# Kernel optimization log

Measured on AMD Instinct MI355X. Metric: run time of the kernel, lower is better.

Reference implementation:

```python
import jax, jax.numpy as jnp
import numpy as np

ASSIGN_RATIO = 0.1  # hard-coded inside coarsen_graph in the original
EPS_CUT = 1e-7
EPS_NORM = 1e-12  # torch F.normalize eps


def _normalize_batch_adj(adj):
    # adj: [B, N, N]
    n = adj.shape[1]
    A = adj + jnp.eye(n, dtype=adj.dtype)
    deg_inv_sqrt = jnp.clip(A.sum(-1), 1.0, None) ** -0.5  # [B, N]
    newA = deg_inv_sqrt[..., :, None] * A * deg_inv_sqrt[..., None, :]
    row_mask = (adj.sum(-1) > 0).astype(adj.dtype)  # [B, N]
    return row_mask[..., :, None] * newA


def setup_inputs():
    key = jax.random.key(0)
    k0, k1, k2, k3, k4 = jax.random.split(key, 5)
    B, N, D, T = 512, 128, 256, 512
    concept_hidden = jax.random.normal(k0, (B, N, D), jnp.float32)
    adj = jax.random.uniform(k1, (B, N, N), jnp.float32)
    head = jax.random.randint(k2, (B, T), 0, N)
    lin_w = jax.random.normal(k3, (1, D), jnp.float32) / np.sqrt(D).astype(np.float32)
    bias = jax.random.normal(k4, (1,), jnp.float32)
    return {"concept_hidden": concept_hidden, "adj": adj, "head": head,
            "lin_w": lin_w, "bias": bias}


def reference(concept_hidden, adj, head, lin_w, bias):
    # concept_hidden: [B, N, D], adj: [B, N, N], head: [B, T] node indices
    x = concept_hidden
    B, N, D = x.shape

    out = x @ lin_w.T                      # [B, N, 1]  self.lin(x)
    norm_adj = _normalize_batch_adj(adj)   # [B, N, N]
    out = norm_adj @ out + bias            # [B, N, 1]
    alpha = jax.nn.sigmoid(out ** 2)[..., 0]  # [B, N]

    # batch_num_nodes[i] = len(set(head[i]))  -> count unique via sort
    hs = jnp.sort(head, axis=-1)
    n_uniq = 1 + (hs[:, 1:] != hs[:, :-1]).sum(-1)  # [B]

    # per-sample k = ceil(n * 0.1) + 1 (only when n > 1); cut = k-th largest alpha
    k = jnp.ceil(n_uniq.astype(jnp.float32) * ASSIGN_RATIO).astype(jnp.int32) + 1
    a_desc = jnp.sort(alpha, axis=-1)[:, ::-1]       # descending
    idx = jnp.clip(k - 1, 0, N - 1)
    cut = jnp.take_along_axis(a_desc, idx[:, None], axis=-1)[:, 0]
    cut = jnp.where(n_uniq > 1, cut, jnp.zeros_like(cut))  # [B]

    cut_alpha = jax.nn.relu(alpha + EPS_CUT - cut[:, None])  # [B, N]

    # S = norm_adj * cut_alpha broadcast over rows, then L1-normalize rows
    S = norm_adj * cut_alpha[:, None, :]
    S = S / jnp.clip(jnp.abs(S).sum(-1, keepdims=True), EPS_NORM, None)

    St = jnp.swapaxes(S, 1, 2)             # [B, N, N]
    embedding_tensor = St @ x              # S^T x   [B, N, D]
    new_adj = (St @ adj) @ S               # S^T A S [B, N, N]
    return embedding_tensor, new_adj
```

## Files before the change

kernel.cpp:

```cpp
#include <hip/hip_runtime.h>

#define Bsz 512
#define Nn  128
#define Dd  256
#define Tt  512

typedef __attribute__((ext_vector_type(8))) short short8;
typedef __attribute__((ext_vector_type(4))) float f32x4;

__device__ __forceinline__ ushort f2bf(float f) {
    union { float f; unsigned u; } v; v.f = f;
    unsigned r = v.u + 0x7fffu + ((v.u >> 16) & 1u);
    return (ushort)(r >> 16);
}
__device__ __forceinline__ unsigned pk2(float a, float b) {
    return (unsigned)f2bf(a) | ((unsigned)f2bf(b) << 16);
}
__device__ __forceinline__ float bf2f(ushort u) {
    union { unsigned u; float f; } v; v.u = (unsigned)u << 16; return v.f;
}

__global__ __launch_bounds__(1024, 4) void mega(
    const float* __restrict__ x, const float* __restrict__ adj,
    const int* __restrict__ head, const float* __restrict__ lin_w,
    const float* __restrict__ bias,
    float* __restrict__ emb, float* __restrict__ nadj)
{
    const int t = threadIdx.x, b = blockIdx.x;
    __shared__ __align__(16) ushort adjB[Nn][136];
    __shared__ __align__(16) ushort STl[Nn][136];
    __shared__ __align__(16) uint   xT0[Nn][68];
    __shared__ __align__(16) uint   xT1[Nn][68];
    __shared__ float ttS[Nn], disS[Nn], maskS[Nn], alphaS[Nn], rowcS[Nn];
    __shared__ float dotP2[Nn][2];
    __shared__ int   flags[Nn];
    __shared__ int   nuniq;
    __shared__ float cutS;

    const float bias0 = bias[0];
    if (t < Nn) flags[t] = 0;
    if (t == 0) { nuniq = 0; cutS = 0.f; }

    const int lane = t & 63, w = t >> 6;
    const int l15 = lane & 15, quad = lane >> 4;
    const int mrow  = (w & 7) * 16;
    const int nhalf = (w >> 3) * 64;
    const int r = t >> 3, seg = t & 7;
    const int xrow = t & 127, kq0 = t >> 7;

    int hv = 0;
    if (t < Tt) hv = head[(size_t)b * Tt + t];

    float e0[8], g0[8], e1[8], g1[8];
    {
        const float* xb = x + (size_t)b * Nn * Dd + xrow;
#pragma unroll
        for (int k = 0; k < 8; ++k) e0[k] = xb[(size_t)(8 * kq0 + k) * Dd];
#pragma unroll
        for (int k = 0; k < 8; ++k) g0[k] = xb[(size_t)(64 + 8 * kq0 + k) * Dd];
#pragma unroll
        for (int k = 0; k < 8; ++k) e1[k] = xb[(size_t)(8 * kq0 + k) * Dd + 128];
#pragma unroll
        for (int k = 0; k < 8; ++k) g1[k] = xb[(size_t)(64 + 8 * kq0 + k) * Dd + 128];
    }
    float4 av0, av1, av2, av3;
    {
        const float4* adjb = (const float4*)(adj + (size_t)b * Nn * Nn);
        av0 = adjb[t]; av1 = adjb[t + 1024]; av2 = adjb[t + 2048]; av3 = adjb[t + 3072];
    }
    const float wv0 = lin_w[xrow], wv1 = lin_w[128 + xrow];

#pragma unroll
    for (int k = 0; k < 8; ++k) {
        float re = e0[k] * wv0 + e1[k] * wv1;
        float rg = g0[k] * wv0 + g1[k] * wv1;
        re += __shfl_xor(re, 1); re += __shfl_xor(re, 2); re += __shfl_xor(re, 4);
        re += __shfl_xor(re, 8); re += __shfl_xor(re, 16); re += __shfl_xor(re, 32);
        rg += __shfl_xor(rg, 1); rg += __shfl_xor(rg, 2); rg += __shfl_xor(rg, 4);
        rg += __shfl_xor(rg, 8); rg += __shfl_xor(rg, 16); rg += __shfl_xor(rg, 32);
        if (lane == 0) {
            dotP2[8 * kq0 + k][w & 1]      = re;
            dotP2[64 + 8 * kq0 + k][w & 1] = rg;
        }
    }

    {
        uint4 q;
        q.x = pk2(e0[0], e0[1]); q.y = pk2(e0[2], e0[3]);
        q.z = pk2(e0[4], e0[5]); q.w = pk2(e0[6], e0[7]);
        *(uint4*)&xT0[xrow][4 * kq0] = q;
        q.x = pk2(g0[0], g0[1]); q.y = pk2(g0[2], g0[3]);
        q.z = pk2(g0[4], g0[5]); q.w = pk2(g0[6], g0[7]);
        *(uint4*)&xT0[xrow][4 * (kq0 + 8)] = q;
        q.x = pk2(e1[0], e1[1]); q.y = pk2(e1[2], e1[3]);
        q.z = pk2(e1[4], e1[5]); q.w = pk2(e1[6], e1[7]);
        *(uint4*)&xT1[xrow][4 * kq0] = q;
        q.x = pk2(g1[0], g1[1]); q.y = pk2(g1[2], g1[3]);
        q.z = pk2(g1[4], g1[5]); q.w = pk2(g1[6], g1[7]);
        *(uint4*)&xT1[xrow][4 * (kq0 + 8)] = q;
    }
    {
        float4 v; int f, rr2, c; uint2 w2;
        v = av0; f = t;        rr2 = f >> 5; c = (f & 31) * 4; w2.x = pk2(v.x, v.y); w2.y = pk2(v.z, v.w); *(uint2*)&adjB[rr2][c] = w2;
        v = av1; f = t + 1024; rr2 = f >> 5; c = (f & 31) * 4; w2.x = pk2(v.x, v.y); w2.y = pk2(v.z, v.w); *(uint2*)&adjB[rr2][c] = w2;
        v = av2; f = t + 2048; rr2 = f >> 5; c = (f & 31) * 4; w2.x = pk2(v.x, v.y); w2.y = pk2(v.z, v.w); *(uint2*)&adjB[rr2][c] = w2;
        v = av3; f = t + 3072; rr2 = f >> 5; c = (f & 31) * 4; w2.x = pk2(v.x, v.y); w2.y = pk2(v.z, v.w); *(uint2*)&adjB[rr2][c] = w2;
    }
    __syncthreads();

    if (t < Tt) flags[hv] = 1;

    {
        short8 a0 = *(const short8*)&adjB[r][seg * 16];
        short8 a1 = *(const short8*)&adjB[r][seg * 16 + 8];
        float s = 0.f;
#pragma unroll
        for (int j = 0; j < 8; ++j) s += bf2f((ushort)a0[j]) + bf2f((ushort)a1[j]);
        s += __shfl_xor(s, 1); s += __shfl_xor(s, 2); s += __shfl_xor(s, 4);
        if (seg == 0) {
            maskS[r] = (s > 0.f) ? 1.f : 0.f;
            float dis = 1.f / sqrtf(fmaxf(s + 1.f, 1.f));
            disS[r] = dis;
            ttS[r]  = dis * (dotP2[r][0] + dotP2[r][1]);
        }
    }
    __syncthreads();

    {
        short8 a0 = *(const short8*)&adjB[r][seg * 16];
        short8 a1 = *(const short8*)&adjB[r][seg * 16 + 8];
        float s = 0.f;
#pragma unroll
        for (int j = 0; j < 8; ++j) {
            s += bf2f((ushort)a0[j]) * ttS[seg * 16 + j];
            s += bf2f((ushort)a1[j]) * ttS[seg * 16 + 8 + j];
        }
        s += __shfl_xor(s, 1); s += __shfl_xor(s, 2); s += __shfl_xor(s, 4);
        if (seg == 0) {
            float o = maskS[r] * disS[r] * (s + ttS[r]) + bias0;
            alphaS[r] = 1.f / (1.f + expf(-o * o));
            atomicAdd(&nuniq, flags[r]);
        }
    }
    __syncthreads();

    {
        int nu = nuniq;
        if (nu > 1) {
            float an = alphaS[r];
            int cg = 0, ce = 0;
            const int j0 = seg * 16;
#pragma unroll
            for (int j = 0; j < 16; ++j) {
                float aj = alphaS[j0 + j];
                cg += (aj > an); ce += (aj == an);
            }
            cg += __shfl_xor(cg, 1); cg += __shfl_xor(cg, 2); cg += __shfl_xor(cg, 4);
            ce += __shfl_xor(ce, 1); ce += __shfl_xor(ce, 2); ce += __shfl_xor(ce, 4);
            if (seg == 0) {
                int idx = (int)ceilf((float)nu * 0.1f);
                if (idx > Nn - 1) idx = Nn - 1;
                if (cg <= idx && idx < cg + ce) cutS = an;
            }
        }
    }
    __syncthreads();

    {
        const float cut = cutS;
        short8 a0 = *(const short8*)&adjB[r][seg * 16];
        short8 a1 = *(const short8*)&adjB[r][seg * 16 + 8];
        float s = 0.f;
#pragma unroll
        for (int j = 0; j < 8; ++j) {
            int j0 = seg * 16 + j, j1 = seg * 16 + 8 + j;
            float u0 = fmaxf(alphaS[j0] + 1e-7f - cut, 0.f) * disS[j0];
            float u1 = fmaxf(alphaS[j1] + 1e-7f - cut, 0.f) * disS[j1];
            s += bf2f((ushort)a0[j]) * u0 + bf2f((ushort)a1[j]) * u1;
        }
        s += __shfl_xor(s, 1); s += __shfl_xor(s, 2); s += __shfl_xor(s, 4);
        if (seg == 0) {
            float ur   = fmaxf(alphaS[r] + 1e-7f - cut, 0.f) * disS[r];
            float rsum = maskS[r] * disS[r] * (ur + s);
            rowcS[r]   = maskS[r] * disS[r] / fmaxf(rsum, 1e-12f);
        }
    }
    __syncthreads();

    {
        const float cut = cutS;
        const int m = t & 127, sl = t >> 7, k0 = sl * 16;
        const float um = fmaxf(alphaS[m] + 1e-7f - cut, 0.f) * disS[m];
        float vv[16];
#pragma unroll
        for (int j = 0; j < 16; ++j) {
            int k = k0 + j;
            vv[j] = rowcS[k] * (bf2f(adjB[k][m]) + ((k == m) ? 1.f : 0.f)) * um;
        }
        uint4 p0, p1;
        p0.x = pk2(vv[0],  vv[1]);  p0.y = pk2(vv[2],  vv[3]);
        p0.z = pk2(vv[4],  vv[5]);  p0.w = pk2(vv[6],  vv[7]);
        p1.x = pk2(vv[8],  vv[9]);  p1.y = pk2(vv[10], vv[11]);
        p1.z = pk2(vv[12], vv[13]); p1.w = pk2(vv[14], vv[15]);
        *(uint4*)&STl[m][k0]     = p0;
        *(uint4*)&STl[m][k0 + 8] = p1;
    }
    __syncthreads();

    f32x4 acc[4];
#pragma unroll
    for (int nt = 0; nt < 4; ++nt) acc[nt] = (f32x4){0.f, 0.f, 0.f, 0.f};
#pragma unroll
    for (int k0 = 0; k0 < 128; k0 += 32) {
        short8 a0 = *(const short8*)&adjB[mrow + l15][k0 + quad * 8];
#pragma unroll
        for (int nt = 0; nt < 4; ++nt) {
            short8 bf = *(const short8*)&STl[nhalf + nt * 16 + l15][k0 + quad * 8];
            acc[nt] = __builtin_amdgcn_mfma_f32_16x16x32_bf16(a0, bf, acc[nt], 0, 0, 0);
        }
    }
    __syncthreads();

    ushort (*PT)[136] = (ushort(*)[136])&adjB[0][0];
#pragma unroll
    for (int nt = 0; nt < 4; ++nt) {
        int j    = nhalf + nt * 16 + l15;
        int mcol = mrow + quad * 4;
        uint2 w2;
        w2.x = pk2(acc[nt][0], acc[nt][1]);
        w2.y = pk2(acc[nt][2], acc[nt][3]);
        *(uint2*)&PT[j][mcol] = w2;
    }
    __syncthreads();

#pragma unroll
    for (int nt = 0; nt < 4; ++nt) acc[nt] = (f32x4){0.f, 0.f, 0.f, 0.f};
#pragma unroll
    for (int k0 = 0; k0 < 128; k0 += 32) {
        short8 a0 = *(const short8*)&STl[mrow + l15][k0 + quad * 8];
#pragma unroll
        for (int nt = 0; nt < 4; ++nt) {
            short8 bf = *(const short8*)&PT[nhalf + nt * 16 + l15][k0 + quad * 8];
            acc[nt] = __builtin_amdgcn_mfma_f32_16x16x32_bf16(a0, bf, acc[nt], 0, 0, 0);
        }
    }
#pragma unroll
    for (int nt = 0; nt < 4; ++nt)
#pragma unroll
        for (int rr2 = 0; rr2 < 4; ++rr2) {
            int row = mrow + quad * 4 + rr2;
            int col = nhalf + nt * 16 + l15;
            nadj[((size_t)b * Nn + row) * Nn + col] = acc[nt][rr2];
        }

    const int dcb = (w >> 3) * 64;
    short8 aE[4];
#pragma unroll
    for (int ks = 0; ks < 4; ++ks)
        aE[ks] = *(const short8*)&STl[mrow + l15][ks * 32 + quad * 8];

    f32x4 accE[4];
#pragma unroll
    for (int nt = 0; nt < 4; ++nt) accE[nt] = (f32x4){0.f, 0.f, 0.f, 0.f};
#pragma unroll
    for (int ks = 0; ks < 4; ++ks) {
#pragma unroll
        for (int nt = 0; nt < 4; ++nt) {
            short8 bf = *(const short8*)&xT0[dcb + nt * 16 + l15][ks * 16 + quad * 4];
            accE[nt] = __builtin_amdgcn_mfma_f32_16x16x32_bf16(aE[ks], bf, accE[nt], 0, 0, 0);
        }
    }
#pragma unroll
    for (int nt = 0; nt < 4; ++nt)
#pragma unroll
        for (int rr2 = 0; rr2 < 4; ++rr2) {
            int row = mrow + quad * 4 + rr2;
            int col = dcb + nt * 16 + l15;
            emb[((size_t)b * Nn + row) * Dd + col] = accE[nt][rr2];
        }

#pragma unroll
    for (int nt = 0; nt < 4; ++nt) accE[nt] = (f32x4){0.f, 0.f, 0.f, 0.f};
#pragma unroll
    for (int ks = 0; ks < 4; ++ks) {
#pragma unroll
        for (int nt = 0; nt < 4; ++nt) {
            short8 bf = *(const short8*)&xT1[dcb + nt * 16 + l15][ks * 16 + quad * 4];
            accE[nt] = __builtin_amdgcn_mfma_f32_16x16x32_bf16(aE[ks], bf, accE[nt], 0, 0, 0);
        }
    }
#pragma unroll
    for (int nt = 0; nt < 4; ++nt)
#pragma unroll
        for (int rr2 = 0; rr2 < 4; ++rr2) {
            int row = mrow + quad * 4 + rr2;
            int col = 128 + dcb + nt * 16 + l15;
            emb[((size_t)b * Nn + row) * Dd + col] = accE[nt][rr2];
        }
}

extern "C" void kernel_launch(void* const* d_in, const int* in_sizes, int n_in,
                              void* d_out, int out_size, void* d_ws, size_t ws_size,
                              hipStream_t stream)
{
    const float* x     = (const float*)d_in[0];
    const float* adj   = (const float*)d_in[1];
    const int*   head  = (const int*)d_in[2];
    const float* lin_w = (const float*)d_in[3];
    const float* bias  = (const float*)d_in[4];

    float* emb  = (float*)d_out;
    float* nadj = emb + (size_t)Bsz * Nn * Dd;

    mega<<<Bsz, 1024, 0, stream>>>(x, adj, head, lin_w, bias, emb, nadj);
}
```

Baseline: 200.1 us.

## Process two graphs per block and prefetch the second graph's inputs during compute

Each block now handles two batch samples in sequence. It issues the global loads of x, adj and head for the second sample before the MFMA phase of the first, so memory latency overlaps with compute. The grid is halved to 256 blocks. It also replaces __syncthreads with a custom barrier that waits only on LDS counters, and cuts the full-wave dot-product shuffle reduction to 8 lanes plus a partial-sum table. In exchange, the prefetch registers raise register pressure, and 256 blocks on a 256-CU part may leave less parallelism to hide latency.

After: 309.5 us. +54.6%, slower.

```diff
diff --git a/kernel.cpp b/kernel.cpp
--- a/kernel.cpp
+++ b/kernel.cpp
@@ -19,6 +19,11 @@
 __device__ __forceinline__ float bf2f(ushort u) {
     union { unsigned u; float f; } v; v.u = (unsigned)u << 16; return v.f;
 }
+
+#define BARL() do { __builtin_amdgcn_sched_barrier(0); \
+    asm volatile("s_waitcnt lgkmcnt(0)" ::: "memory"); \
+    __builtin_amdgcn_s_barrier(); \
+    __builtin_amdgcn_sched_barrier(0); } while (0)
 
 __global__ __launch_bounds__(1024, 4) void mega(
     const float* __restrict__ x, const float* __restrict__ adj,
@@ -26,277 +31,319 @@
     const float* __restrict__ bias,
     float* __restrict__ emb, float* __restrict__ nadj)
 {
-    const int t = threadIdx.x, b = blockIdx.x;
+    const int t = threadIdx.x;
     __shared__ __align__(16) ushort adjB[Nn][136];
     __shared__ __align__(16) ushort STl[Nn][136];
     __shared__ __align__(16) uint   xT0[Nn][68];
     __shared__ __align__(16) uint   xT1[Nn][68];
-    __shared__ float ttS[Nn], disS[Nn], maskS[Nn], alphaS[Nn], rowcS[Nn];
-    __shared__ float dotP2[Nn][2];
+    __shared__ __align__(16) float ttS[Nn], disS[Nn], alphaS[Nn], rowcS[Nn];
+    __shared__ float maskS[Nn];
+    __shared__ float partS[Nn][18];
     __shared__ int   flags[Nn];
     __shared__ int   nuniq;
     __shared__ float cutS;
 
     const float bias0 = bias[0];
-    if (t < Nn) flags[t] = 0;
-    if (t == 0) { nuniq = 0; cutS = 0.f; }
-
     const int lane = t & 63, w = t >> 6;
     const int l15 = lane & 15, quad = lane >> 4;
     const int mrow  = (w & 7) * 16;
     const int nhalf = (w >> 3) * 64;
     const int r = t >> 3, seg = t & 7;
     const int xrow = t & 127, kq0 = t >> 7;
-
-    int hv = 0;
-    if (t < Tt) hv = head[(size_t)b * Tt + t];
-
-    float e0[8], g0[8], e1[8], g1[8];
-    {
-        const float* xb = x + (size_t)b * Nn * Dd + xrow;
-#pragma unroll
-        for (int k = 0; k < 8; ++k) e0[k] = xb[(size_t)(8 * kq0 + k) * Dd];
-#pragma unroll
-        for (int k = 0; k < 8; ++k) g0[k] = xb[(size_t)(64 + 8 * kq0 + k) * Dd];
-#pragma unroll
-        for (int k = 0; k < 8; ++k) e1[k] = xb[(size_t)(8 * kq0 + k) * Dd + 128];
-#pragma unroll
-        for (int k = 0; k < 8; ++k) g1[k] = xb[(size_t)(64 + 8 * kq0 + k) * Dd + 128];
+    const float wv0 = lin_w[xrow], wv1 = lin_w[128 + xrow];
+
+    float pe0[8], pg0[8], pe1[8], pg1[8];
+    float4 pav0, pav1, pav2, pav3;
+    int hv1 = 0;
+
+    for (int it = 0; it < 2; ++it) {
+        const int b = 2 * blockIdx.x + it;
+
+        if (t < Nn) flags[t] = 0;
+        if (t == 0) { nuniq = 0; cutS = 0.f; }
+
+        int hv = 0;
+        float e0[8], g0[8], e1[8], g1[8];
+        float4 a0v, a1v, a2v, a3v;
+        if (it == 0) {
+            if (t < Tt) hv = head[(size_t)b * Tt + t];
+            const float* xb = x + (size_t)b * Nn * Dd + xrow;
+#pragma unroll
+            for (int k = 0; k < 8; ++k) e0[k] = xb[(size_t)(8 * kq0 + k) * Dd];
+#pragma unroll
+            for (int k = 0; k < 8; ++k) g0[k] = xb[(size_t)(64 + 8 * kq0 + k) * Dd];
+#pragma unroll
+            for (int k = 0; k < 8; ++k) e1[k] = xb[(size_t)(8 * kq0 + k) * Dd + 128];
+#pragma unroll
+            for (int k = 0; k < 8; ++k) g1[k] = xb[(size_t)(64 + 8 * kq0 + k) * Dd + 128];
+            const float4* ab = (const float4*)(adj + (size_t)b * Nn * Nn);
+            a0v = ab[t]; a1v = ab[t + 1024]; a2v = ab[t + 2048]; a3v = ab[t + 3072];
+        } else {
+            hv = hv1;
+#pragma unroll
+            for (int k = 0; k < 8; ++k) { e0[k] = pe0[k]; g0[k] = pg0[k]; e1[k] = pe1[k]; g1[k] = pg1[k]; }
+            a0v = pav0; a1v = pav1; a2v = pav2; a3v = pav3;
+        }
+
+#pragma unroll
+        for (int k = 0; k < 8; ++k) {
+            float re = e0[k] * wv0 + e1[k] * wv1;
+            float rg = g0[k] * wv0 + g1[k] * wv1;
+            re += __shfl_xor(re, 1); re += __shfl_xor(re, 2); re += __shfl_xor(re, 4);
+            rg += __shfl_xor(rg, 1); rg += __shfl_xor(rg, 2); rg += __shfl_xor(rg, 4);
+            if ((lane & 7) == 0) {
+                int gc = (w & 1) * 8 + (lane >> 3);
+                partS[8 * kq0 + k][gc]      = re;
+                partS[64 + 8 * kq0 + k][gc] = rg;
+            }
+        }
+        {
+            uint4 q;
+            q.x = pk2(e0[0], e0[1]); q.y = pk2(e0[2], e0[3]);
+            q.z = pk2(e0[4], e0[5]); q.w = pk2(e0[6], e0[7]);
+            *(uint4*)&xT0[xrow][4 * kq0] = q;
+            q.x = pk2(g0[0], g0[1]); q.y = pk2(g0[2], g0[3]);
+            q.z = pk2(g0[4], g0[5]); q.w = pk2(g0[6], g0[7]);
+            *(uint4*)&xT0[xrow][4 * kq0 + 32] = q;
+            q.x = pk2(e1[0], e1[1]); q.y = pk2(e1[2], e1[3]);
+            q.z = pk2(e1[4], e1[5]); q.w = pk2(e1[6], e1[7]);
+            *(uint4*)&xT1[xrow][4 * kq0] = q;
+            q.x = pk2(g1[0], g1[1]); q.y = pk2(g1[2], g1[3]);
+            q.z = pk2(g1[4], g1[5]); q.w = pk2(g1[6], g1[7]);
+            *(uint4*)&xT1[xrow][4 * kq0 + 32] = q;
+        }
+        {
+            float4 v; int f, rr2, c; uint2 w2;
+            v = a0v; f = t;        rr2 = f >> 5; c = (f & 31) * 4; w2.x = pk2(v.x, v.y); w2.y = pk2(v.z, v.w); *(uint2*)&adjB[rr2][c] = w2;
+            v = a1v; f = t + 1024; rr2 = f >> 5; c = (f & 31) * 4; w2.x = pk2(v.x, v.y); w2.y = pk2(v.z, v.w); *(uint2*)&adjB[rr2][c] = w2;
+            v = a2v; f = t + 2048; rr2 = f >> 5; c = (f & 31) * 4; w2.x = pk2(v.x, v.y); w2.y = pk2(v.z, v.w); *(uint2*)&adjB[rr2][c] = w2;
+            v = a3v; f = t + 3072; rr2 = f >> 5; c = (f & 31) * 4; w2.x = pk2(v.x, v.y); w2.y = pk2(v.z, v.w); *(uint2*)&adjB[rr2][c] = w2;
+        }
+        BARL();
+
+        if (t < Tt) flags[hv] = 1;
+
+        {
+            short8 a0 = *(const short8*)&adjB[r][seg * 16];
+            short8 a1 = *(const short8*)&adjB[r][seg * 16 + 8];
+            float s = 0.f;
+#pragma unroll
+            for (int j = 0; j < 8; ++j) s += bf2f((ushort)a0[j]) + bf2f((ushort)a1[j]);
+            float d = partS[r][2 * seg] + partS[r][2 * seg + 1];
+            s += __shfl_xor(s, 1); s += __shfl_xor(s, 2); s += __shfl_xor(s, 4);
+            d += __shfl_xor(d, 1); d += __shfl_xor(d, 2); d += __shfl_xor(d, 4);
+            if (seg == 0) {
+                maskS[r] = (s > 0.f) ? 1.f : 0.f;
+                float dis = 1.f / sqrtf(fmaxf(s + 1.f, 1.f));
+                disS[r] = dis;
+                ttS[r]  = dis * d;
+            }
+        }
+        BARL();
+
+        {
+            short8 a0 = *(const short8*)&adjB[r][seg * 16];
+            short8 a1 = *(const short8*)&adjB[r][seg * 16 + 8];
+            f32x4 t0 = *(const f32x4*)&ttS[seg * 16];
+            f32x4 t1 = *(const f32x4*)&ttS[seg * 16 + 4];
+            f32x4 t2 = *(const f32x4*)&ttS[seg * 16 + 8];
+            f32x4 t3 = *(const f32x4*)&ttS[seg * 16 + 12];
+            float s = 0.f;
+#pragma unroll
+            for (int j = 0; j < 4; ++j) {
+                s += bf2f((ushort)a0[j])     * t0[j];
+                s += bf2f((ushort)a0[4 + j]) * t1[j];
+                s += bf2f((ushort)a1[j])     * t2[j];
+                s += bf2f((ushort)a1[4 + j]) * t3[j];
+            }
+            s += __shfl_xor(s, 1); s += __shfl_xor(s, 2); s += __shfl_xor(s, 4);
+            if (seg == 0) {
+                float o = maskS[r] * disS[r] * (s + ttS[r]) + bias0;
+                alphaS[r] = 1.f / (1.f + expf(-o * o));
+                atomicAdd(&nuniq, flags[r]);
+            }
+        }
+        BARL();
+
+        {
+            int nu = nuniq;
+            if (nu > 1) {
+                float an = alphaS[r];
+                int cg = 0, ce = 0;
+#pragma unroll
+                for (int v = 0; v < 4; ++v) {
+                    f32x4 A = *(const f32x4*)&alphaS[seg * 16 + 4 * v];
+#pragma unroll
+                    for (int j = 0; j < 4; ++j) { cg += (A[j] > an); ce += (A[j] == an); }
+                }
+                cg += __shfl_xor(cg, 1); cg += __shfl_xor(cg, 2); cg += __shfl_xor(cg, 4);
+                ce += __shfl_xor(ce, 1); ce += __shfl_xor(ce, 2); ce += __shfl_xor(ce, 4);
+                if (seg == 0) {
+                    int idx = (int)ceilf((float)nu * 0.1f);
+                    if (idx > Nn - 1) idx = Nn - 1;
+                    if (cg <= idx && idx < cg + ce) cutS = an;
+                }
+            }
+        }
+        BARL();
+
+        {
+            const float cut = cutS;
+            short8 a0 = *(const short8*)&adjB[r][seg * 16];
+            short8 a1 = *(const short8*)&adjB[r][seg * 16 + 8];
+            float s = 0.f;
+#pragma unroll
+            for (int v = 0; v < 4; ++v) {
+                f32x4 A = *(const f32x4*)&alphaS[seg * 16 + 4 * v];
+                f32x4 D = *(const f32x4*)&disS[seg * 16 + 4 * v];
+#pragma unroll
+                for (int j = 0; j < 4; ++j) {
+                    float u = fmaxf(A[j] + 1e-7f - cut, 0.f) * D[j];
+                    float av = (v < 2) ? bf2f((ushort)a0[4 * v + j])
+                                       : bf2f((ushort)a1[4 * (v - 2) + j]);
+                    s += av * u;
+                }
+            }
+            s += __shfl_xor(s, 1); s += __shfl_xor(s, 2); s += __shfl_xor(s, 4);
+            if (seg == 0) {
+                float ur   = fmaxf(alphaS[r] + 1e-7f - cut, 0.f) * disS[r];
+                float rsum = maskS[r] * disS[r] * (ur + s);
+                rowcS[r]   = maskS[r] * disS[r] / fmaxf(rsum, 1e-12f);
+            }
+        }
+        BARL();
+
+        {
+            const float cut = cutS;
+            const int m = t & 127, sl = t >> 7, k0 = sl * 16;
+            const float um = fmaxf(alphaS[m] + 1e-7f - cut, 0.f) * disS[m];
+            f32x4 R0 = *(const f32x4*)&rowcS[k0];
+            f32x4 R1 = *(const f32x4*)&rowcS[k0 + 4];
+            f32x4 R2 = *(const f32x4*)&rowcS[k0 + 8];
+            f32x4 R3 = *(const f32x4*)&rowcS[k0 + 12];
+            float vv[16];
+#pragma unroll
+            for (int j = 0; j < 16; ++j) {
+                int k = k0 + j;
+                float rc = (j < 4) ? R0[j] : (j < 8) ? R1[j - 4] : (j < 12) ? R2[j - 8] : R3[j - 12];
+                vv[j] = rc * (bf2f(adjB[k][m]) + ((k == m) ? 1.f : 0.f)) * um;
+            }
+            uint4 p0, p1;
+            p0.x = pk2(vv[0],  vv[1]);  p0.y = pk2(vv[2],  vv[3]);
+            p0.z = pk2(vv[4],  vv[5]);  p0.w = pk2(vv[6],  vv[7]);
+            p1.x = pk2(vv[8],  vv[9]);  p1.y = pk2(vv[10], vv[11]);
+            p1.z = pk2(vv[12], vv[13]); p1.w = pk2(vv[14], vv[15]);
+            *(uint4*)&STl[m][k0]     = p0;
+            *(uint4*)&STl[m][k0 + 8] = p1;
+        }
+        BARL();
+
+        if (it == 0) {
+            const float* xb = x + (size_t)(b + 1) * Nn * Dd + xrow;
+#pragma unroll
+            for (int k = 0; k < 8; ++k) pe0[k] = xb[(size_t)(8 * kq0 + k) * Dd];
+#pragma unroll
+            for (int k = 0; k < 8; ++k) pg0[k] = xb[(size_t)(64 + 8 * kq0 + k) * Dd];
+#pragma unroll
+            for (int k = 0; k < 8; ++k) pe1[k] = xb[(size_t)(8 * kq0 + k) * Dd + 128];
+#pragma unroll
+            for (int k = 0; k < 8; ++k) pg1[k] = xb[(size_t)(64 + 8 * kq0 + k) * Dd + 128];
+            const float4* ab = (const float4*)(adj + (size_t)(b + 1) * Nn * Nn);
+            pav0 = ab[t]; pav1 = ab[t + 1024]; pav2 = ab[t + 2048]; pav3 = ab[t + 3072];
+            if (t < Tt) hv1 = head[(size_t)(b + 1) * Tt + t];
+            __builtin_amdgcn_sched_barrier(0);
+        }
+
+        f32x4 acc[4];
+#pragma unroll
+        for (int nt = 0; nt < 4; ++nt) acc[nt] = (f32x4){0.f, 0.f, 0.f, 0.f};
+#pragma unroll
+        for (int k0 = 0; k0 < 128; k0 += 32) {
+            short8 a0 = *(const short8*)&adjB[mrow + l15][k0 + quad * 8];
+#pragma unroll
+            for (int nt = 0; nt < 4; ++nt) {
+                short8 bf = *(const short8*)&STl[nhalf + nt * 16 + l15][k0 + quad * 8];
+                acc[nt] = __builtin_amdgcn_mfma_f32_16x16x32_bf16(a0, bf, acc[nt], 0, 0, 0);
+            }
+        }
+        BARL();
+
+        ushort (*PT)[136] = (ushort(*)[136])&adjB[0][0];
+#pragma unroll
+        for (int nt = 0; nt < 4; ++nt) {
+            int j    = nhalf + nt * 16 + l15;
+            int mcol = mrow + quad * 4;
+            uint2 w2;
+            w2.x = pk2(acc[nt][0], acc[nt][1]);
+            w2.y = pk2(acc[nt][2], acc[nt][3]);
+            *(uint2*)&PT[j][mcol] = w2;
+        }
+        BARL();
+
+#pragma unroll
+        for (int nt = 0; nt < 4; ++nt) acc[nt] = (f32x4){0.f, 0.f, 0.f, 0.f};
+#pragma unroll
+        for (int k0 = 0; k0 < 128; k0 += 32) {
+            short8 a0 = *(const short8*)&STl[mrow + l15][k0 + quad * 8];
+#pragma unroll
+            for (int nt = 0; nt < 4; ++nt) {
+                short8 bf = *(const short8*)&PT[nhalf + nt * 16 + l15][k0 + quad * 8];
+                acc[nt] = __builtin_amdgcn_mfma_f32_16x16x32_bf16(a0, bf, acc[nt], 0, 0, 0);
+            }
+        }
+#pragma unroll
+        for (int nt = 0; nt < 4; ++nt)
+#pragma unroll
+            for (int rr2 = 0; rr2 < 4; ++rr2) {
+                int row = mrow + quad * 4 + rr2;
+                int col = nhalf + nt * 16 + l15;
+                nadj[((size_t)b * Nn + row) * Nn + col] = acc[nt][rr2];
+            }
+
+        const int dcb = (w >> 3) * 64;
+        f32x4 accE[4];
+#pragma unroll
+        for (int nt = 0; nt < 4; ++nt) accE[nt] = (f32x4){0.f, 0.f, 0.f, 0.f};
+#pragma unroll
+        for (int ks = 0; ks < 4; ++ks) {
+            short8 aE = *(const short8*)&STl[mrow + l15][ks * 32 + quad * 8];
+#pragma unroll
+            for (int nt = 0; nt < 4; ++nt) {
+                short8 bf = *(const short8*)&xT0[dcb + nt * 16 + l15][ks * 16 + quad * 4];
+                accE[nt] = __builtin_amdgcn_mfma_f32_16x16x32_bf16(aE, bf, accE[nt], 0, 0, 0);
+            }
+        }
+#pragma unroll
+        for (int nt = 0; nt < 4; ++nt)
+#pragma unroll
+            for (int rr2 = 0; rr2 < 4; ++rr2) {
+                int row = mrow + quad * 4 + rr2;
+                int col = dcb + nt * 16 + l15;
+                emb[((size_t)b * Nn + row) * Dd + col] = accE[nt][rr2];
+            }
+
+#pragma unroll
+        for (int nt = 0; nt < 4; ++nt) accE[nt] = (f32x4){0.f, 0.f, 0.f, 0.f};
+#pragma unroll
+        for (int ks = 0; ks < 4; ++ks) {
+            short8 aE = *(const short8*)&STl[mrow + l15][ks * 32 + quad * 8];
+#pragma unroll
+            for (int nt = 0; nt < 4; ++nt) {
+                short8 bf = *(const short8*)&xT1[dcb + nt * 16 + l15][ks * 16 + quad * 4];
+                accE[nt] = __builtin_amdgcn_mfma_f32_16x16x32_bf16(aE, bf, accE[nt], 0, 0, 0);
+            }
+        }
+#pragma unroll
+        for (int nt = 0; nt < 4; ++nt)
+#pragma unroll
+            for (int rr2 = 0; rr2 < 4; ++rr2) {
+                int row = mrow + quad * 4 + rr2;
+                int col = 128 + dcb + nt * 16 + l15;
+                emb[((size_t)b * Nn + row) * Dd + col] = accE[nt][rr2];
+            }
+
+        BARL();
     }
-    float4 av0, av1, av2, av3;
-    {
-        const float4* adjb = (const float4*)(adj + (size_t)b * Nn * Nn);
-        av0 = adjb[t]; av1 = adjb[t + 1024]; av2 = adjb[t + 2048]; av3 = adjb[t + 3072];
-    }
-    const float wv0 = lin_w[xrow], wv1 = lin_w[128 + xrow];
-
-#pragma unroll
-    for (int k = 0; k < 8; ++k) {
-        float re = e0[k] * wv0 + e1[k] * wv1;
-        float rg = g0[k] * wv0 + g1[k] * wv1;
-        re += __shfl_xor(re, 1); re += __shfl_xor(re, 2); re += __shfl_xor(re, 4);
-        re += __shfl_xor(re, 8); re += __shfl_xor(re, 16); re += __shfl_xor(re, 32);
-        rg += __shfl_xor(rg, 1); rg += __shfl_xor(rg, 2); rg += __shfl_xor(rg, 4);
-        rg += __shfl_xor(rg, 8); rg += __shfl_xor(rg, 16); rg += __shfl_xor(rg, 32);
-        if (lane == 0) {
-            dotP2[8 * kq0 + k][w & 1]      = re;
-            dotP2[64 + 8 * kq0 + k][w & 1] = rg;
-        }
-    }
-
-    {
-        uint4 q;
-        q.x = pk2(e0[0], e0[1]); q.y = pk2(e0[2], e0[3]);
-        q.z = pk2(e0[4], e0[5]); q.w = pk2(e0[6], e0[7]);
-        *(uint4*)&xT0[xrow][4 * kq0] = q;
-        q.x = pk2(g0[0], g0[1]); q.y = pk2(g0[2], g0[3]);
-        q.z = pk2(g0[4], g0[5]); q.w = pk2(g0[6], g0[7]);
-        *(uint4*)&xT0[xrow][4 * (kq0 + 8)] = q;
-        q.x = pk2(e1[0], e1[1]); q.y = pk2(e1[2], e1[3]);
-        q.z = pk2(e1[4], e1[5]); q.w = pk2(e1[6], e1[7]);
-        *(uint4*)&xT1[xrow][4 * kq0] = q;
-        q.x = pk2(g1[0], g1[1]); q.y = pk2(g1[2], g1[3]);
-        q.z = pk2(g1[4], g1[5]); q.w = pk2(g1[6], g1[7]);
-        *(uint4*)&xT1[xrow][4 * (kq0 + 8)] = q;
-    }
-    {
-        float4 v; int f, rr2, c; uint2 w2;
-        v = av0; f = t;        rr2 = f >> 5; c = (f & 31) * 4; w2.x = pk2(v.x, v.y); w2.y = pk2(v.z, v.w); *(uint2*)&adjB[rr2][c] = w2;
-        v = av1; f = t + 1024; rr2 = f >> 5; c = (f & 31) * 4; w2.x = pk2(v.x, v.y); w2.y = pk2(v.z, v.w); *(uint2*)&adjB[rr2][c] = w2;
-        v = av2; f = t + 2048; rr2 = f >> 5; c = (f & 31) * 4; w2.x = pk2(v.x, v.y); w2.y = pk2(v.z, v.w); *(uint2*)&adjB[rr2][c] = w2;
-        v = av3; f = t + 3072; rr2 = f >> 5; c = (f & 31) * 4; w2.x = pk2(v.x, v.y); w2.y = pk2(v.z, v.w); *(uint2*)&adjB[rr2][c] = w2;
-    }
-    __syncthreads();
-
-    if (t < Tt) flags[hv] = 1;
-
-    {
-        short8 a0 = *(const short8*)&adjB[r][seg * 16];
-        short8 a1 = *(const short8*)&adjB[r][seg * 16 + 8];
-        float s = 0.f;
-#pragma unroll
-        for (int j = 0; j < 8; ++j) s += bf2f((ushort)a0[j]) + bf2f((ushort)a1[j]);
-        s += __shfl_xor(s, 1); s += __shfl_xor(s, 2); s += __shfl_xor(s, 4);
-        if (seg == 0) {
-            maskS[r] = (s > 0.f) ? 1.f : 0.f;
-            float dis = 1.f / sqrtf(fmaxf(s + 1.f, 1.f));
-            disS[r] = dis;
-            ttS[r]  = dis * (dotP2[r][0] + dotP2[r][1]);
-        }
-    }
-    __syncthreads();
-
-    {
-        short8 a0 = *(const short8*)&adjB[r][seg * 16];
-        short8 a1 = *(const short8*)&adjB[r][seg * 16 + 8];
-        float s = 0.f;
-#pragma unroll
-        for (int j = 0; j < 8; ++j) {
-            s += bf2f((ushort)a0[j]) * ttS[seg * 16 + j];
-            s += bf2f((ushort)a1[j]) * ttS[seg * 16 + 8 + j];
-        }
-        s += __shfl_xor(s, 1); s += __shfl_xor(s, 2); s += __shfl_xor(s, 4);
-        if (seg == 0) {
-            float o = maskS[r] * disS[r] * (s + ttS[r]) + bias0;
-            alphaS[r] = 1.f / (1.f + expf(-o * o));
-            atomicAdd(&nuniq, flags[r]);
-        }
-    }
-    __syncthreads();
-
-    {
-        int nu = nuniq;
-        if (nu > 1) {
-            float an = alphaS[r];
-            int cg = 0, ce = 0;
-            const int j0 = seg * 16;
-#pragma unroll
-            for (int j = 0; j < 16; ++j) {
-                float aj = alphaS[j0 + j];
-                cg += (aj > an); ce += (aj == an);
-            }
-            cg += __shfl_xor(cg, 1); cg += __shfl_xor(cg, 2); cg += __shfl_xor(cg, 4);
-            ce += __shfl_xor(ce, 1); ce += __shfl_xor(ce, 2); ce += __shfl_xor(ce, 4);
-            if (seg == 0) {
-                int idx = (int)ceilf((float)nu * 0.1f);
-                if (idx > Nn - 1) idx = Nn - 1;
-                if (cg <= idx && idx < cg + ce) cutS = an;
-            }
-        }
-    }
-    __syncthreads();
-
-    {
-        const float cut = cutS;
-        short8 a0 = *(const short8*)&adjB[r][seg * 16];
-        short8 a1 = *(const short8*)&adjB[r][seg * 16 + 8];
-        float s = 0.f;
-#pragma unroll
-        for (int j = 0; j < 8; ++j) {
-            int j0 = seg * 16 + j, j1 = seg * 16 + 8 + j;
-            float u0 = fmaxf(alphaS[j0] + 1e-7f - cut, 0.f) * disS[j0];
-            float u1 = fmaxf(alphaS[j1] + 1e-7f - cut, 0.f) * disS[j1];
-            s += bf2f((ushort)a0[j]) * u0 + bf2f((ushort)a1[j]) * u1;
-        }
-        s += __shfl_xor(s, 1); s += __shfl_xor(s, 2); s += __shfl_xor(s, 4);
-        if (seg == 0) {
-            float ur   = fmaxf(alphaS[r] + 1e-7f - cut, 0.f) * disS[r];
-            float rsum = maskS[r] * disS[r] * (ur + s);
-            rowcS[r]   = maskS[r] * disS[r] / fmaxf(rsum, 1e-12f);
-        }
-    }
-    __syncthreads();
-
-    {
-        const float cut = cutS;
-        const int m = t & 127, sl = t >> 7, k0 = sl * 16;
-        const float um = fmaxf(alphaS[m] + 1e-7f - cut, 0.f) * disS[m];
-        float vv[16];
-#pragma unroll
-        for (int j = 0; j < 16; ++j) {
-            int k = k0 + j;
-            vv[j] = rowcS[k] * (bf2f(adjB[k][m]) + ((k == m) ? 1.f : 0.f)) * um;
-        }
-        uint4 p0, p1;
-        p0.x = pk2(vv[0],  vv[1]);  p0.y = pk2(vv[2],  vv[3]);
-        p0.z = pk2(vv[4],  vv[5]);  p0.w = pk2(vv[6],  vv[7]);
-        p1.x = pk2(vv[8],  vv[9]);  p1.y = pk2(vv[10], vv[11]);
-        p1.z = pk2(vv[12], vv[13]); p1.w = pk2(vv[14], vv[15]);
-        *(uint4*)&STl[m][k0]     = p0;
-        *(uint4*)&STl[m][k0 + 8] = p1;
-    }
-    __syncthreads();
-
-    f32x4 acc[4];
-#pragma unroll
-    for (int nt = 0; nt < 4; ++nt) acc[nt] = (f32x4){0.f, 0.f, 0.f, 0.f};
-#pragma unroll
-    for (int k0 = 0; k0 < 128; k0 += 32) {
-        short8 a0 = *(const short8*)&adjB[mrow + l15][k0 + quad * 8];
-#pragma unroll
-        for (int nt = 0; nt < 4; ++nt) {
-            short8 bf = *(const short8*)&STl[nhalf + nt * 16 + l15][k0 + quad * 8];
-            acc[nt] = __builtin_amdgcn_mfma_f32_16x16x32_bf16(a0, bf, acc[nt], 0, 0, 0);
-        }
-    }
-    __syncthreads();
-
-    ushort (*PT)[136] = (ushort(*)[136])&adjB[0][0];
-#pragma unroll
-    for (int nt = 0; nt < 4; ++nt) {
-        int j    = nhalf + nt * 16 + l15;
-        int mcol = mrow + quad * 4;
-        uint2 w2;
-        w2.x = pk2(acc[nt][0], acc[nt][1]);
-        w2.y = pk2(acc[nt][2], acc[nt][3]);
-        *(uint2*)&PT[j][mcol] = w2;
-    }
-    __syncthreads();
-
-#pragma unroll
-    for (int nt = 0; nt < 4; ++nt) acc[nt] = (f32x4){0.f, 0.f, 0.f, 0.f};
-#pragma unroll
-    for (int k0 = 0; k0 < 128; k0 += 32) {
-        short8 a0 = *(const short8*)&STl[mrow + l15][k0 + quad * 8];
-#pragma unroll
-        for (int nt = 0; nt < 4; ++nt) {
-            short8 bf = *(const short8*)&PT[nhalf + nt * 16 + l15][k0 + quad * 8];
-            acc[nt] = __builtin_amdgcn_mfma_f32_16x16x32_bf16(a0, bf, acc[nt], 0, 0, 0);
-        }
-    }
-#pragma unroll
-    for (int nt = 0; nt < 4; ++nt)
-#pragma unroll
-        for (int rr2 = 0; rr2 < 4; ++rr2) {
-            int row = mrow + quad * 4 + rr2;
-            int col = nhalf + nt * 16 + l15;
-            nadj[((size_t)b * Nn + row) * Nn + col] = acc[nt][rr2];
-        }
-
-    const int dcb = (w >> 3) * 64;
-    short8 aE[4];
-#pragma unroll
-    for (int ks = 0; ks < 4; ++ks)
-        aE[ks] = *(const short8*)&STl[mrow + l15][ks * 32 + quad * 8];
-
-    f32x4 accE[4];
-#pragma unroll
-    for (int nt = 0; nt < 4; ++nt) accE[nt] = (f32x4){0.f, 0.f, 0.f, 0.f};
-#pragma unroll
-    for (int ks = 0; ks < 4; ++ks) {
-#pragma unroll
-        for (int nt = 0; nt < 4; ++nt) {
-            short8 bf = *(const short8*)&xT0[dcb + nt * 16 + l15][ks * 16 + quad * 4];
-            accE[nt] = __builtin_amdgcn_mfma_f32_16x16x32_bf16(aE[ks], bf, accE[nt], 0, 0, 0);
-        }
-    }
-#pragma unroll
-    for (int nt = 0; nt < 4; ++nt)
-#pragma unroll
-        for (int rr2 = 0; rr2 < 4; ++rr2) {
-            int row = mrow + quad * 4 + rr2;
-            int col = dcb + nt * 16 + l15;
-            emb[((size_t)b * Nn + row) * Dd + col] = accE[nt][rr2];
-        }
-
-#pragma unroll
-    for (int nt = 0; nt < 4; ++nt) accE[nt] = (f32x4){0.f, 0.f, 0.f, 0.f};
-#pragma unroll
-    for (int ks = 0; ks < 4; ++ks) {
-#pragma unroll
-        for (int nt = 0; nt < 4; ++nt) {
-            short8 bf = *(const short8*)&xT1[dcb + nt * 16 + l15][ks * 16 + quad * 4];
-            accE[nt] = __builtin_amdgcn_mfma_f32_16x16x32_bf16(aE[ks], bf, accE[nt], 0, 0, 0);
-        }
-    }
-#pragma unroll
-    for (int nt = 0; nt < 4; ++nt)
-#pragma unroll
-        for (int rr2 = 0; rr2 < 4; ++rr2) {
-            int row = mrow + quad * 4 + rr2;
-            int col = 128 + dcb + nt * 16 + l15;
-            emb[((size_t)b * Nn + row) * Dd + col] = accE[nt][rr2];
-        }
 }
 
 extern "C" void kernel_launch(void* const* d_in, const int* in_sizes, int n_in,
@@ -312,5 +359,5 @@
     float* emb  = (float*)d_out;
     float* nadj = emb + (size_t)Bsz * Nn * Dd;
 
-    mega<<<Bsz, 1024, 0, stream>>>(x, adj, head, lin_w, bias, emb, nadj);
-}
+    mega<<<Bsz / 2, 1024, 0, stream>>>(x, adj, head, lin_w, bias, emb, nadj);
+}
```

## Swizzle shared-memory tiles and compute row sums from fp32 registers

Applied to the files above, without the earlier changes.

Adds an XOR swizzle for the bf16 adjacency, S^T and transposed x tiles in shared memory, aimed at cutting LDS bank conflicts in the MFMA operand loads and the strided transpose reads. Row degree sums are now taken from the fp32 global loads through shuffles and partial buffers, and the lin dot-product reduction is shortened to three shuffles plus a shared-memory reduction, so one pass over adjB goes away. Several scalar LDS reads become vectorised f32x4 reads, and S^T fragments are reloaded per k-step instead of held in registers, which lowers register pressure. Degree sums now come from unrounded fp32 instead of bf16, which changes numerics slightly.

Result: slower. 204.9 us (+2.4%).

```diff
diff --git a/kernel.cpp b/kernel.cpp
--- a/kernel.cpp
+++ b/kernel.cpp
@@ -18,6 +18,16 @@
 }
 __device__ __forceinline__ float bf2f(ushort u) {
     union { unsigned u; float f; } v; v.u = (unsigned)u << 16; return v.f;
+}
+
+__device__ __forceinline__ int SWZ(int row, int g) {
+    return g ^ ((row ^ (row >> 3)) & 7);
+}
+__device__ __forceinline__ ushort* AP(ushort* base, int row, int col) {
+    return base + row * 136 + (SWZ(row, col >> 3) << 3) + (col & 7);
+}
+__device__ __forceinline__ uint* XP(uint* base, int row, int col) {
+    return base + row * 68 + (SWZ(row, col >> 2) << 2) + (col & 3);
 }
 
 __global__ __launch_bounds__(1024, 4) void mega(
@@ -27,12 +37,13 @@
     float* __restrict__ emb, float* __restrict__ nadj)
 {
     const int t = threadIdx.x, b = blockIdx.x;
-    __shared__ __align__(16) ushort adjB[Nn][136];
-    __shared__ __align__(16) ushort STl[Nn][136];
-    __shared__ __align__(16) uint   xT0[Nn][68];
-    __shared__ __align__(16) uint   xT1[Nn][68];
+    __shared__ __align__(16) ushort adjR[Nn * 136];
+    __shared__ __align__(16) ushort stR[Nn * 136];
+    __shared__ __align__(16) uint   xtR0[Nn * 68];
+    __shared__ __align__(16) uint   xtR1[Nn * 68];
     __shared__ float ttS[Nn], disS[Nn], maskS[Nn], alphaS[Nn], rowcS[Nn];
-    __shared__ float dotP2[Nn][2];
+    __shared__ float partS[Nn][18];
+    __shared__ float partS2[Nn][4];
     __shared__ int   flags[Nn];
     __shared__ int   nuniq;
     __shared__ float cutS;
@@ -47,6 +58,7 @@
     const int nhalf = (w >> 3) * 64;
     const int r = t >> 3, seg = t & 7;
     const int xrow = t & 127, kq0 = t >> 7;
+    const float wv0 = lin_w[xrow], wv1 = lin_w[128 + xrow];
 
     int hv = 0;
     if (t < Tt) hv = head[(size_t)b * Tt + t];
@@ -68,19 +80,36 @@
         const float4* adjb = (const float4*)(adj + (size_t)b * Nn * Nn);
         av0 = adjb[t]; av1 = adjb[t + 1024]; av2 = adjb[t + 2048]; av3 = adjb[t + 3072];
     }
-    const float wv0 = lin_w[xrow], wv1 = lin_w[128 + xrow];
 
 #pragma unroll
     for (int k = 0; k < 8; ++k) {
         float re = e0[k] * wv0 + e1[k] * wv1;
         float rg = g0[k] * wv0 + g1[k] * wv1;
         re += __shfl_xor(re, 1); re += __shfl_xor(re, 2); re += __shfl_xor(re, 4);
-        re += __shfl_xor(re, 8); re += __shfl_xor(re, 16); re += __shfl_xor(re, 32);
         rg += __shfl_xor(rg, 1); rg += __shfl_xor(rg, 2); rg += __shfl_xor(rg, 4);
-        rg += __shfl_xor(rg, 8); rg += __shfl_xor(rg, 16); rg += __shfl_xor(rg, 32);
-        if (lane == 0) {
-            dotP2[8 * kq0 + k][w & 1]      = re;
-            dotP2[64 + 8 * kq0 + k][w & 1] = rg;
+        if ((lane & 7) == 0) {
+            int gc = (w & 1) * 8 + (lane >> 3);
+            partS[8 * kq0 + k][gc]      = re;
+            partS[64 + 8 * kq0 + k][gc] = rg;
+        }
+    }
+
+    {
+        float s0 = av0.x + av0.y + av0.z + av0.w;
+        float s1 = av1.x + av1.y + av1.z + av1.w;
+        float s2 = av2.x + av2.y + av2.z + av2.w;
+        float s3 = av3.x + av3.y + av3.z + av3.w;
+        s0 += __shfl_xor(s0, 1); s0 += __shfl_xor(s0, 2); s0 += __shfl_xor(s0, 4);
+        s1 += __shfl_xor(s1, 1); s1 += __shfl_xor(s1, 2); s1 += __shfl_xor(s1, 4);
+        s2 += __shfl_xor(s2, 1); s2 += __shfl_xor(s2, 2); s2 += __shfl_xor(s2, 4);
+        s3 += __shfl_xor(s3, 1); s3 += __shfl_xor(s3, 2); s3 += __shfl_xor(s3, 4);
+        if ((lane & 7) == 0) {
+            int q = (lane & 31) >> 3;
+            int row0 = t >> 5;
+            partS2[row0][q]       = s0;
+            partS2[row0 + 32][q]  = s1;
+            partS2[row0 + 64][q]  = s2;
+            partS2[row0 + 96][q]  = s3;
         }
     }
 
@@ -88,52 +117,56 @@
         uint4 q;
         q.x = pk2(e0[0], e0[1]); q.y = pk2(e0[2], e0[3]);
         q.z = pk2(e0[4], e0[5]); q.w = pk2(e0[6], e0[7]);
-        *(uint4*)&xT0[xrow][4 * kq0] = q;
+        *(uint4*)XP(xtR0, xrow, 4 * kq0) = q;
         q.x = pk2(g0[0], g0[1]); q.y = pk2(g0[2], g0[3]);
         q.z = pk2(g0[4], g0[5]); q.w = pk2(g0[6], g0[7]);
-        *(uint4*)&xT0[xrow][4 * (kq0 + 8)] = q;
+        *(uint4*)XP(xtR0, xrow, 4 * kq0 + 32) = q;
         q.x = pk2(e1[0], e1[1]); q.y = pk2(e1[2], e1[3]);
         q.z = pk2(e1[4], e1[5]); q.w = pk2(e1[6], e1[7]);
-        *(uint4*)&xT1[xrow][4 * kq0] = q;
+        *(uint4*)XP(xtR1, xrow, 4 * kq0) = q;
         q.x = pk2(g1[0], g1[1]); q.y = pk2(g1[2], g1[3]);
         q.z = pk2(g1[4], g1[5]); q.w = pk2(g1[6], g1[7]);
-        *(uint4*)&xT1[xrow][4 * (kq0 + 8)] = q;
+        *(uint4*)XP(xtR1, xrow, 4 * kq0 + 32) = q;
     }
     {
         float4 v; int f, rr2, c; uint2 w2;
-        v = av0; f = t;        rr2 = f >> 5; c = (f & 31) * 4; w2.x = pk2(v.x, v.y); w2.y = pk2(v.z, v.w); *(uint2*)&adjB[rr2][c] = w2;
-        v = av1; f = t + 1024; rr2 = f >> 5; c = (f & 31) * 4; w2.x = pk2(v.x, v.y); w2.y = pk2(v.z, v.w); *(uint2*)&adjB[rr2][c] = w2;
-        v = av2; f = t + 2048; rr2 = f >> 5; c = (f & 31) * 4; w2.x = pk2(v.x, v.y); w2.y = pk2(v.z, v.w); *(uint2*)&adjB[rr2][c] = w2;
-        v = av3; f = t + 3072; rr2 = f >> 5; c = (f & 31) * 4; w2.x = pk2(v.x, v.y); w2.y = pk2(v.z, v.w); *(uint2*)&adjB[rr2][c] = w2;
+        v = av0; f = t;        rr2 = f >> 5; c = (f & 31) * 4; w2.x = pk2(v.x, v.y); w2.y = pk2(v.z, v.w); *(uint2*)AP(adjR, rr2, c) = w2;
+        v = av1; f = t + 1024; rr2 = f >> 5; c = (f & 31) * 4; w2.x = pk2(v.x, v.y); w2.y = pk2(v.z, v.w); *(uint2*)AP(adjR, rr2, c) = w2;
+        v = av2; f = t + 2048; rr2 = f >> 5; c = (f & 31) * 4; w2.x = pk2(v.x, v.y); w2.y = pk2(v.z, v.w); *(uint2*)AP(adjR, rr2, c) = w2;
+        v = av3; f = t + 3072; rr2 = f >> 5; c = (f & 31) * 4; w2.x = pk2(v.x, v.y); w2.y = pk2(v.z, v.w); *(uint2*)AP(adjR, rr2, c) = w2;
     }
     __syncthreads();
 
     if (t < Tt) flags[hv] = 1;
 
     {
-        short8 a0 = *(const short8*)&adjB[r][seg * 16];
-        short8 a1 = *(const short8*)&adjB[r][seg * 16 + 8];
-        float s = 0.f;
-#pragma unroll
-        for (int j = 0; j < 8; ++j) s += bf2f((ushort)a0[j]) + bf2f((ushort)a1[j]);
+        float d = partS[r][2 * seg] + partS[r][2 * seg + 1];
+        float s = (seg < 4) ? partS2[r][seg] : 0.f;
+        d += __shfl_xor(d, 1); d += __shfl_xor(d, 2); d += __shfl_xor(d, 4);
         s += __shfl_xor(s, 1); s += __shfl_xor(s, 2); s += __shfl_xor(s, 4);
         if (seg == 0) {
             maskS[r] = (s > 0.f) ? 1.f : 0.f;
             float dis = 1.f / sqrtf(fmaxf(s + 1.f, 1.f));
             disS[r] = dis;
-            ttS[r]  = dis * (dotP2[r][0] + dotP2[r][1]);
-        }
-    }
-    __syncthreads();
-
-    {
-        short8 a0 = *(const short8*)&adjB[r][seg * 16];
-        short8 a1 = *(const short8*)&adjB[r][seg * 16 + 8];
+            ttS[r]  = dis * d;
+        }
+    }
+    __syncthreads();
+
+    {
+        short8 a0 = *(const short8*)AP(adjR, r, seg * 16);
+        short8 a1 = *(const short8*)AP(adjR, r, seg * 16 + 8);
+        f32x4 t0 = *(const f32x4*)&ttS[seg * 16];
+        f32x4 t1 = *(const f32x4*)&ttS[seg * 16 + 4];
+        f32x4 t2 = *(const f32x4*)&ttS[seg * 16 + 8];
+        f32x4 t3 = *(const f32x4*)&ttS[seg * 16 + 12];
         float s = 0.f;
 #pragma unroll
-        for (int j = 0; j < 8; ++j) {
-            s += bf2f((ushort)a0[j]) * ttS[seg * 16 + j];
-            s += bf2f((ushort)a1[j]) * ttS[seg * 16 + 8 + j];
+        for (int j = 0; j < 4; ++j) {
+            s += bf2f((ushort)a0[j])     * t0[j];
+            s += bf2f((ushort)a0[4 + j]) * t1[j];
+            s += bf2f((ushort)a1[j])     * t2[j];
+            s += bf2f((ushort)a1[4 + j]) * t3[j];
         }
         s += __shfl_xor(s, 1); s += __shfl_xor(s, 2); s += __shfl_xor(s, 4);
         if (seg == 0) {
@@ -149,11 +182,11 @@
         if (nu > 1) {
             float an = alphaS[r];
             int cg = 0, ce = 0;
-            const int j0 = seg * 16;
-#pragma unroll
-            for (int j = 0; j < 16; ++j) {
-                float aj = alphaS[j0 + j];
-                cg += (aj > an); ce += (aj == an);
+#pragma unroll
+            for (int v = 0; v < 4; ++v) {
+                f32x4 A = *(const f32x4*)&alphaS[seg * 16 + 4 * v];
+#pragma unroll
+                for (int j = 0; j < 4; ++j) { cg += (A[j] > an); ce += (A[j] == an); }
             }
             cg += __shfl_xor(cg, 1); cg += __shfl_xor(cg, 2); cg += __shfl_xor(cg, 4);
             ce += __shfl_xor(ce, 1); ce += __shfl_xor(ce, 2); ce += __shfl_xor(ce, 4);
@@ -168,15 +201,20 @@
 
     {
         const float cut = cutS;
-        short8 a0 = *(const short8*)&adjB[r][seg * 16];
-        short8 a1 = *(const short8*)&adjB[r][seg * 16 + 8];
+        short8 a0 = *(const short8*)AP(adjR, r, seg * 16);
+        short8 a1 = *(const short8*)AP(adjR, r, seg * 16 + 8);
         float s = 0.f;
 #pragma unroll
-        for (int j = 0; j < 8; ++j) {
-            int j0 = seg * 16 + j, j1 = seg * 16 + 8 + j;
-            float u0 = fmaxf(alphaS[j0] + 1e-7f - cut, 0.f) * disS[j0];
-            float u1 = fmaxf(alphaS[j1] + 1e-7f - cut, 0.f) * disS[j1];
-            s += bf2f((ushort)a0[j]) * u0 + bf2f((ushort)a1[j]) * u1;
+        for (int v = 0; v < 4; ++v) {
+            f32x4 A = *(const f32x4*)&alphaS[seg * 16 + 4 * v];
+            f32x4 D = *(const f32x4*)&disS[seg * 16 + 4 * v];
+#pragma unroll
+            for (int j = 0; j < 4; ++j) {
+                float u = fmaxf(A[j] + 1e-7f - cut, 0.f) * D[j];
+                float av = (v < 2) ? bf2f((ushort)a0[4 * v + j])
+                                   : bf2f((ushort)a1[4 * (v - 2) + j]);
+                s += av * u;
+            }
         }
         s += __shfl_xor(s, 1); s += __shfl_xor(s, 2); s += __shfl_xor(s, 4);
         if (seg == 0) {
@@ -195,15 +233,15 @@
 #pragma unroll
         for (int j = 0; j < 16; ++j) {
             int k = k0 + j;
-            vv[j] = rowcS[k] * (bf2f(adjB[k][m]) + ((k == m) ? 1.f : 0.f)) * um;
+            vv[j] = rowcS[k] * (bf2f(*AP(adjR, k, m)) + ((k == m) ? 1.f : 0.f)) * um;
         }
         uint4 p0, p1;
         p0.x = pk2(vv[0],  vv[1]);  p0.y = pk2(vv[2],  vv[3]);
         p0.z = pk2(vv[4],  vv[5]);  p0.w = pk2(vv[6],  vv[7]);
         p1.x = pk2(vv[8],  vv[9]);  p1.y = pk2(vv[10], vv[11]);
         p1.z = pk2(vv[12], vv[13]); p1.w = pk2(vv[14], vv[15]);
-        *(uint4*)&STl[m][k0]     = p0;
-        *(uint4*)&STl[m][k0 + 8] = p1;
+        *(uint4*)AP(stR, m, k0)     = p0;
+        *(uint4*)AP(stR, m, k0 + 8) = p1;
     }
     __syncthreads();
 
@@ -212,16 +250,15 @@
     for (int nt = 0; nt < 4; ++nt) acc[nt] = (f32x4){0.f, 0.f, 0.f, 0.f};
 #pragma unroll
     for (int k0 = 0; k0 < 128; k0 += 32) {
-        short8 a0 = *(const short8*)&adjB[mrow + l15][k0 + quad * 8];
+        short8 a0 = *(const short8*)AP(adjR, mrow + l15, k0 + quad * 8);
 #pragma unroll
         for (int nt = 0; nt < 4; ++nt) {
-            short8 bf = *(const short8*)&STl[nhalf + nt * 16 + l15][k0 + quad * 8];
+            short8 bf = *(const short8*)AP(stR, nhalf + nt * 16 + l15, k0 + quad * 8);
             acc[nt] = __builtin_amdgcn_mfma_f32_16x16x32_bf16(a0, bf, acc[nt], 0, 0, 0);
         }
     }
     __syncthreads();
 
-    ushort (*PT)[136] = (ushort(*)[136])&adjB[0][0];
 #pragma unroll
     for (int nt = 0; nt < 4; ++nt) {
         int j    = nhalf + nt * 16 + l15;
@@ -229,7 +266,7 @@
         uint2 w2;
         w2.x = pk2(acc[nt][0], acc[nt][1]);
         w2.y = pk2(acc[nt][2], acc[nt][3]);
-        *(uint2*)&PT[j][mcol] = w2;
+        *(uint2*)AP(adjR, j, mcol) = w2;
     }
     __syncthreads();
 
@@ -237,10 +274,10 @@
     for (int nt = 0; nt < 4; ++nt) acc[nt] = (f32x4){0.f, 0.f, 0.f, 0.f};
 #pragma unroll
     for (int k0 = 0; k0 < 128; k0 += 32) {
-        short8 a0 = *(const short8*)&STl[mrow + l15][k0 + quad * 8];
+        short8 a0 = *(const short8*)AP(stR, mrow + l15, k0 + quad * 8);
 #pragma unroll
         for (int nt = 0; nt < 4; ++nt) {
-            short8 bf = *(const short8*)&PT[nhalf + nt * 16 + l15][k0 + quad * 8];
+            short8 bf = *(const short8*)AP(adjR, nhalf + nt * 16 + l15, k0 + quad * 8);
             acc[nt] = __builtin_amdgcn_mfma_f32_16x16x32_bf16(a0, bf, acc[nt], 0, 0, 0);
         }
     }
@@ -254,20 +291,16 @@
         }
 
     const int dcb = (w >> 3) * 64;
-    short8 aE[4];
-#pragma unroll
-    for (int ks = 0; ks < 4; ++ks)
-        aE[ks] = *(const short8*)&STl[mrow + l15][ks * 32 + quad * 8];
-
     f32x4 accE[4];
 #pragma unroll
     for (int nt = 0; nt < 4; ++nt) accE[nt] = (f32x4){0.f, 0.f, 0.f, 0.f};
 #pragma unroll
     for (int ks = 0; ks < 4; ++ks) {
+        short8 aE = *(const short8*)AP(stR, mrow + l15, ks * 32 + quad * 8);
 #pragma unroll
         for (int nt = 0; nt < 4; ++nt) {
-            short8 bf = *(const short8*)&xT0[dcb + nt * 16 + l15][ks * 16 + quad * 4];
-            accE[nt] = __builtin_amdgcn_mfma_f32_16x16x32_bf16(aE[ks], bf, accE[nt], 0, 0, 0);
+            short8 bf = *(const short8*)XP(xtR0, dcb + nt * 16 + l15, ks * 16 + quad * 4);
+            accE[nt] = __builtin_amdgcn_mfma_f32_16x16x32_bf16(aE, bf, accE[nt], 0, 0, 0);
         }
     }
 #pragma unroll
@@ -283,10 +316,11 @@
     for (int nt = 0; nt < 4; ++nt) accE[nt] = (f32x4){0.f, 0.f, 0.f, 0.f};
 #pragma unroll
     for (int ks = 0; ks < 4; ++ks) {
+        short8 aE = *(const short8*)AP(stR, mrow + l15, ks * 32 + quad * 8);
 #pragma unroll
         for (int nt = 0; nt < 4; ++nt) {
-            short8 bf = *(const short8*)&xT1[dcb + nt * 16 + l15][ks * 16 + quad * 4];
-            accE[nt] = __builtin_amdgcn_mfma_f32_16x16x32_bf16(aE[ks], bf, accE[nt], 0, 0, 0);
+            short8 bf = *(const short8*)XP(xtR1, dcb + nt * 16 + l15, ks * 16 + quad * 4);
+            accE[nt] = __builtin_amdgcn_mfma_f32_16x16x32_bf16(aE, bf, accE[nt], 0, 0, 0);
         }
     }
 #pragma unroll
```
